# Performance work log

Hardware: AMD Instinct MI355X
Metric: run time of the kernel (lower is better)

The kernel has to match this reference:

```python
import jax, jax.numpy as jnp
import numpy as np

B, S, D, H = 2, 2048, 1024, 16
DK = D // H


def setup_inputs() -> dict:
    key = jax.random.key(0)
    ks = jax.random.split(key, 6)
    inp = {
        "mha_input": jax.random.normal(ks[0], (B, S, D), dtype=jnp.float32),
        "mask": jax.random.randint(ks[1], (B, S), 0, 2, dtype=jnp.int32),
        "Wq_w": jax.random.normal(ks[2], (D, D), dtype=jnp.float32) * 0.02,
        "Wq_b": jnp.zeros((D,), dtype=jnp.float32),
        "Wk_w": jax.random.normal(ks[3], (D, D), dtype=jnp.float32) * 0.02,
        "Wk_b": jnp.zeros((D,), dtype=jnp.float32),
        "Wv_w": jax.random.normal(ks[4], (D, D), dtype=jnp.float32) * 0.02,
        "Wv_b": jnp.zeros((D,), dtype=jnp.float32),
        "Wo_w": jax.random.normal(ks[5], (D, D), dtype=jnp.float32) * 0.02,
        "Wo_b": jnp.zeros((D,), dtype=jnp.float32),
    }
    return inp


def _mha(x, mask, Wq_w, Wq_b, Wk_w, Wk_b, Wv_w, Wv_b, Wo_w, Wo_b):
    b, s, d = x.shape
    # nn.Linear: x @ W.T + b
    q = (x @ Wq_w.T + Wq_b).reshape(b, s, H, DK).transpose(0, 2, 1, 3)  # [B,H,S,DK]
    k = (x @ Wk_w.T + Wk_b).reshape(b, s, H, DK).transpose(0, 2, 1, 3)
    v = (x @ Wv_w.T + Wv_b).reshape(b, s, H, DK).transpose(0, 2, 1, 3)
    scores = jnp.einsum("bhqd,bhkd->bhqk", q, k) / jnp.sqrt(jnp.float32(DK))
    # prefix mask: key columns < count_nonzero(mask[i]) are kept, rest -inf
    lengths = jnp.count_nonzero(mask, axis=1)                # [B]
    valid = jnp.arange(s)[None, :] < lengths[:, None]        # [B,S]
    scores = jnp.where(valid[:, None, None, :], scores, -jnp.inf)
    attn = jax.nn.softmax(scores, axis=-1)
    out = jnp.einsum("bhqk,bhkd->bhqd", attn, v)             # [B,H,S,DK]
    concat = out.transpose(0, 2, 1, 3).reshape(b, s, d)      # [B,S,D]
    return concat @ Wo_w.T + Wo_b


def reference(mha_input, mask, Wq_w, Wq_b, Wk_w, Wk_b, Wv_w, Wv_b, Wo_w, Wo_b):
    return _mha(mha_input, mask, Wq_w, Wq_b, Wk_w, Wk_b, Wv_w, Wv_b, Wo_w, Wo_b)
```

## Files before the change

### kernel.cpp

```cpp
#include <hip/hip_runtime.h>

using bf16x8 = __attribute__((ext_vector_type(8))) short;
using f32x4  = __attribute__((ext_vector_type(4))) float;

#define S_LEN 2048
#define NHEAD 16
#define DKH   64
#define HSZ   (S_LEN * DKH * 32)

__device__ __forceinline__ unsigned short f2bf(float x) {
  unsigned u = __builtin_bit_cast(unsigned, x);
  u += 0x7FFFu + ((u >> 16) & 1u);
  return (unsigned short)(u >> 16);
}

__device__ __forceinline__ void gload_lds16(const void* g, void* l) {
  __builtin_amdgcn_global_load_lds(
      (const __attribute__((address_space(1))) unsigned int*)g,
      (__attribute__((address_space(3))) unsigned int*)l, 16, 0, 0);
}

__global__ void cvt_kernel(const float* __restrict__ src,
                           unsigned short* __restrict__ dst, int n4) {
  int i = blockIdx.x * blockDim.x + threadIdx.x;
  if (i < n4) {
    float4 v = ((const float4*)src)[i];
    ushort4 o;
    o.x = f2bf(v.x); o.y = f2bf(v.y); o.z = f2bf(v.z); o.w = f2bf(v.w);
    ((ushort4*)dst)[i] = o;
  }
}

__global__ void lens_kernel(const int* __restrict__ mask, int* __restrict__ lens) {
  __shared__ int sred[256];
  const int b = blockIdx.x;
  int c = 0;
  for (int s = threadIdx.x; s < S_LEN; s += 256) c += (mask[b * S_LEN + s] != 0) ? 1 : 0;
  sred[threadIdx.x] = c;
  __syncthreads();
  for (int st = 128; st > 0; st >>= 1) {
    if (threadIdx.x < st) sred[threadIdx.x] += sred[threadIdx.x + st];
    __syncthreads();
  }
  if (threadIdx.x == 0) lens[b] = sred[0];
}

template <int MODE>
__global__ __launch_bounds__(256) void gemm_kernel(
    const unsigned short* __restrict__ A, const unsigned short* __restrict__ B,
    const float* __restrict__ b0, const float* __restrict__ b1,
    const float* __restrict__ b2, unsigned short* __restrict__ outQKV,
    float* __restrict__ outF, const int K) {
  __shared__ __align__(16) unsigned short As[128 * 32];
  __shared__ __align__(16) unsigned short Bs[128 * 32];
  const int tid = threadIdx.x;
  const int w = tid >> 6, lane = tid & 63;
  const int wm = w >> 1, wn = w & 1;
  const int r = lane & 15, g = lane >> 4;
  const int tm = blockIdx.y * 128, tn = blockIdx.x * 128;

  f32x4 acc[4][4] = {};
  const char* Ab = (const char*)A;
  const char* Bb = (const char*)B;
  char* AsB = (char*)As;
  char* BsB = (char*)Bs;

  for (int k0 = 0; k0 < K; k0 += 32) {
#pragma unroll
    for (int i = 0; i < 2; ++i) {
      const int o = (w * 2 + i) * 1024 + lane * 16;
      const int row = o >> 6, colb = o & 63;
      gload_lds16(Ab + ((size_t)(tm + row) * K + k0) * 2 + colb, AsB + (w * 2 + i) * 1024);
      gload_lds16(Bb + ((size_t)(tn + row) * K + k0) * 2 + colb, BsB + (w * 2 + i) * 1024);
    }
    __syncthreads();
    bf16x8 af[4], bfr[4];
#pragma unroll
    for (int mi = 0; mi < 4; ++mi)
      af[mi] = *(const bf16x8*)(AsB + (wm * 64 + mi * 16 + r) * 64 + g * 16);
#pragma unroll
    for (int ni = 0; ni < 4; ++ni)
      bfr[ni] = *(const bf16x8*)(BsB + (wn * 64 + ni * 16 + r) * 64 + g * 16);
#pragma unroll
    for (int mi = 0; mi < 4; ++mi)
#pragma unroll
      for (int ni = 0; ni < 4; ++ni)
        acc[mi][ni] = __builtin_amdgcn_mfma_f32_16x16x32_bf16(af[mi], bfr[ni], acc[mi][ni], 0, 0, 0);
    __syncthreads();
  }

  if (MODE == 0) {
    const int mat = tn >> 10;
    const float* bp = (mat == 0) ? b0 : (mat == 1) ? b1 : b2;
    const float scale = (mat == 0) ? 0.125f : 1.0f;
    unsigned short* dst = outQKV + (size_t)mat * HSZ;
#pragma unroll
    for (int mi = 0; mi < 4; ++mi)
#pragma unroll
      for (int ni = 0; ni < 4; ++ni)
#pragma unroll
        for (int reg = 0; reg < 4; ++reg) {
          const int m = tm + wm * 64 + mi * 16 + 4 * g + reg;
          const int n = tn + wn * 64 + ni * 16 + r;
          const int nn = n & 1023;
          const float v = (acc[mi][ni][reg] + bp[nn]) * scale;
          const int bI = m >> 11, s = m & 2047, hh = nn >> 6, dk = nn & 63;
          dst[(size_t)((bI * NHEAD + hh) * S_LEN + s) * DKH + dk] = f2bf(v);
        }
  } else {
#pragma unroll
    for (int mi = 0; mi < 4; ++mi)
#pragma unroll
      for (int ni = 0; ni < 4; ++ni)
#pragma unroll
        for (int reg = 0; reg < 4; ++reg) {
          const int m = tm + wm * 64 + mi * 16 + 4 * g + reg;
          const int n = tn + wn * 64 + ni * 16 + r;
          outF[(size_t)m * 1024 + n] = acc[mi][ni][reg] + b0[n];
        }
  }
}

__global__ __launch_bounds__(256) void attn_kernel(
    const unsigned short* __restrict__ qkv, const int* __restrict__ lens,
    unsigned short* __restrict__ outc) {
  __shared__ __align__(16) unsigned short Kt[64 * 64];
  __shared__ __align__(16) unsigned short Vt[64 * 64];
  __shared__ __align__(16) unsigned short Pl[4 * 16 * 64];
  const int tid = threadIdx.x;
  const int w = tid >> 6, lane = tid & 63;
  const int r = lane & 15, g = lane >> 4;
  const int bh = blockIdx.y;
  const int b = bh >> 4, h = bh & 15;
  const int q0 = blockIdx.x * 64;

  const unsigned short* Qp = qkv;
  const unsigned short* Kp = qkv + HSZ;
  const unsigned short* Vp = qkv + 2 * (size_t)HSZ;

  const size_t qbase = (size_t)(bh * S_LEN + q0 + w * 16 + r) * DKH;
  const bf16x8 qf0 = *(const bf16x8*)(Qp + qbase + g * 8);
  const bf16x8 qf1 = *(const bf16x8*)(Qp + qbase + 32 + g * 8);

  const int L = lens[b];
  const int nt = (L + 63) >> 6;
  float mrun = -__builtin_inff(), lrun = 0.f;
  f32x4 oacc[4] = {};

  char* KtB = (char*)Kt;
  char* VtB = (char*)Vt;
  char* PlB = (char*)Pl + w * 2048;
  const int swp = (r & 7) << 4;

  for (int t = 0; t < nt; ++t) {
    const int kv0 = t * 64;
    const char* kgb = (const char*)(Kp + (size_t)(bh * S_LEN + kv0) * DKH);
#pragma unroll
    for (int i = 0; i < 2; ++i) {
      const int o = i * 4096 + w * 1024 + lane * 16;
      const int row = o >> 7, colb = o & 127;
      gload_lds16(kgb + row * 128 + (colb ^ ((row & 7) << 4)), KtB + i * 4096 + w * 1024);
    }
    const unsigned short* vgb = Vp + (size_t)(bh * S_LEN + kv0) * DKH;
#pragma unroll
    for (int i = 0; i < 2; ++i) {
      const int u = i * 256 + tid;
      const int c = u & 63, g8 = u >> 6;
      const bf16x8 vv = *(const bf16x8*)(vgb + c * DKH + g8 * 8);
#pragma unroll
      for (int j = 0; j < 8; ++j) {
        const int dk = g8 * 8 + j;
        *(short*)(VtB + dk * 128 + ((2 * c) ^ ((dk & 7) << 4))) = vv[j];
      }
    }
    __syncthreads();

    f32x4 st[4];
#pragma unroll
    for (int f = 0; f < 4; ++f) {
      const int c = f * 16 + r;
      const int sw = (c & 7) << 4;
      const bf16x8 k0 = *(const bf16x8*)(KtB + c * 128 + ((g * 16) ^ sw));
      const bf16x8 k1 = *(const bf16x8*)(KtB + c * 128 + ((64 + g * 16) ^ sw));
      f32x4 a = {};
      a = __builtin_amdgcn_mfma_f32_16x16x32_bf16(k0, qf0, a, 0, 0, 0);
      a = __builtin_amdgcn_mfma_f32_16x16x32_bf16(k1, qf1, a, 0, 0, 0);
      st[f] = a;
    }
    if (t == nt - 1) {
#pragma unroll
      for (int f = 0; f < 4; ++f)
#pragma unroll
        for (int reg = 0; reg < 4; ++reg)
          if (kv0 + f * 16 + 4 * g + reg >= L) st[f][reg] = -__builtin_inff();
    }

    float mloc = st[0][0];
#pragma unroll
    for (int f = 0; f < 4; ++f)
#pragma unroll
      for (int reg = 0; reg < 4; ++reg) mloc = fmaxf(mloc, st[f][reg]);
    mloc = fmaxf(mloc, __shfl_xor(mloc, 16));
    mloc = fmaxf(mloc, __shfl_xor(mloc, 32));
    const float mnew = fmaxf(mrun, mloc);
    const float alpha = __expf(mrun - mnew);
    float psum = 0.f;
#pragma unroll
    for (int f = 0; f < 4; ++f)
#pragma unroll
      for (int reg = 0; reg < 4; ++reg) {
        const float p = __expf(st[f][reg] - mnew);
        st[f][reg] = p;
        psum += p;
      }
    psum += __shfl_xor(psum, 16);
    psum += __shfl_xor(psum, 32);
    lrun = lrun * alpha + psum;
    mrun = mnew;

    float areg[4];
#pragma unroll
    for (int reg = 0; reg < 4; ++reg) areg[reg] = __shfl(alpha, 4 * g + reg);
#pragma unroll
    for (int f = 0; f < 4; ++f)
#pragma unroll
      for (int reg = 0; reg < 4; ++reg) oacc[f][reg] *= areg[reg];

#pragma unroll
    for (int f = 0; f < 4; ++f) {
      ushort4 pw;
      pw.x = f2bf(st[f][0]); pw.y = f2bf(st[f][1]);
      pw.z = f2bf(st[f][2]); pw.w = f2bf(st[f][3]);
      *(ushort4*)(PlB + r * 128 + ((f * 32 + g * 8) ^ swp)) = pw;
    }

#pragma unroll
    for (int c2 = 0; c2 < 2; ++c2) {
      const bf16x8 pa = *(const bf16x8*)(PlB + r * 128 + ((c2 * 64 + g * 16) ^ swp));
#pragma unroll
      for (int f = 0; f < 4; ++f) {
        const int dk = f * 16 + r;
        const bf16x8 vf =
            *(const bf16x8*)(VtB + dk * 128 + ((c2 * 64 + g * 16) ^ ((dk & 7) << 4)));
        oacc[f] = __builtin_amdgcn_mfma_f32_16x16x32_bf16(pa, vf, oacc[f], 0, 0, 0);
      }
    }
    __syncthreads();
  }

  float lreg[4];
#pragma unroll
  for (int reg = 0; reg < 4; ++reg) lreg[reg] = __shfl(lrun, 4 * g + reg);
#pragma unroll
  for (int f = 0; f < 4; ++f) {
    const int dk = f * 16 + r;
#pragma unroll
    for (int reg = 0; reg < 4; ++reg) {
      const int row = 4 * g + reg;
      const float v = oacc[f][reg] / lreg[reg];
      outc[(size_t)(b * S_LEN + q0 + w * 16 + row) * 1024 + h * DKH + dk] = f2bf(v);
    }
  }
}

extern "C" void kernel_launch(void* const* d_in, const int* in_sizes, int n_in,
                              void* d_out, int out_size, void* d_ws, size_t ws_size,
                              hipStream_t stream) {
  const float* x  = (const float*)d_in[0];
  const int* mask = (const int*)d_in[1];
  const float* wq = (const float*)d_in[2];
  const float* bq = (const float*)d_in[3];
  const float* wk = (const float*)d_in[4];
  const float* bk = (const float*)d_in[5];
  const float* wv = (const float*)d_in[6];
  const float* bv = (const float*)d_in[7];
  const float* wo = (const float*)d_in[8];
  const float* bo = (const float*)d_in[9];
  (void)in_sizes; (void)n_in; (void)out_size; (void)ws_size;

  char* ws = (char*)d_ws;
  unsigned short* xb  = (unsigned short*)ws;
  unsigned short* wb  = (unsigned short*)(ws + 8388608);
  unsigned short* wob = (unsigned short*)(ws + 14680064);
  unsigned short* qkv = (unsigned short*)(ws + 16777216);
  unsigned short* ao  = (unsigned short*)(ws + 41943040);
  int* lens           = (int*)(ws + 50331648);
  float* out          = (float*)d_out;

  cvt_kernel<<<4096, 256, 0, stream>>>(x, xb, 1048576);
  cvt_kernel<<<1024, 256, 0, stream>>>(wq, wb, 262144);
  cvt_kernel<<<1024, 256, 0, stream>>>(wk, wb + 1048576, 262144);
  cvt_kernel<<<1024, 256, 0, stream>>>(wv, wb + 2097152, 262144);
  cvt_kernel<<<1024, 256, 0, stream>>>(wo, wob, 262144);
  lens_kernel<<<2, 256, 0, stream>>>(mask, lens);

  gemm_kernel<0><<<dim3(24, 32), 256, 0, stream>>>(xb, wb, bq, bk, bv, qkv, nullptr, 1024);
  attn_kernel<<<dim3(32, 32), 256, 0, stream>>>(qkv, lens, ao);
  gemm_kernel<1><<<dim3(8, 32), 256, 0, stream>>>(ao, wob, bo, nullptr, nullptr, nullptr, out, 1024);
}
```

Baseline: 227.9 us.

## Double-buffer K/V tiles, pre-transpose V in QKV GEMM, process 128 queries per block

The QKV projection now writes V transposed (dk-major), so the attention kernel can load V with async global-to-LDS copies instead of scalar transposing stores. K and V tiles are double-buffered so the next tile's load overlaps the current tile's compute. Each wave handles two 16-row query groups, which reuses K/V fragments and halves the grid. Softmax switches to exp2 with log2e folded into the Q scale, and s_setprio is raised around the MFMA sections. The costs are more LDS, more registers, and only 512 blocks, which lowers occupancy.

Result: faster. 216.6 us (-5.0%).

```diff
diff --git a/kernel.cpp b/kernel.cpp
--- a/kernel.cpp
+++ b/kernel.cpp
@@ -7,6 +7,13 @@
 #define NHEAD 16
 #define DKH   64
 #define HSZ   (S_LEN * DKH * 32)
+#define QSCALE 0.18033688011112042f
+
+#if __has_builtin(__builtin_amdgcn_exp2f)
+#define EXP2(x) __builtin_amdgcn_exp2f(x)
+#else
+#define EXP2(x) exp2f(x)
+#endif
 
 __device__ __forceinline__ unsigned short f2bf(float x) {
   unsigned u = __builtin_bit_cast(unsigned, x);
@@ -92,7 +99,7 @@
   if (MODE == 0) {
     const int mat = tn >> 10;
     const float* bp = (mat == 0) ? b0 : (mat == 1) ? b1 : b2;
-    const float scale = (mat == 0) ? 0.125f : 1.0f;
+    const float scale = (mat == 0) ? QSCALE : 1.0f;
     unsigned short* dst = outQKV + (size_t)mat * HSZ;
 #pragma unroll
     for (int mi = 0; mi < 4; ++mi)
@@ -105,7 +112,11 @@
           const int nn = n & 1023;
           const float v = (acc[mi][ni][reg] + bp[nn]) * scale;
           const int bI = m >> 11, s = m & 2047, hh = nn >> 6, dk = nn & 63;
-          dst[(size_t)((bI * NHEAD + hh) * S_LEN + s) * DKH + dk] = f2bf(v);
+          if (mat == 2) {
+            dst[(size_t)((bI * NHEAD + hh) * DKH + dk) * S_LEN + s] = f2bf(v);
+          } else {
+            dst[(size_t)((bI * NHEAD + hh) * S_LEN + s) * DKH + dk] = f2bf(v);
+          }
         }
   } else {
 #pragma unroll
@@ -121,144 +132,182 @@
   }
 }
 
+__device__ __forceinline__ void online_sm(f32x4* st, float& mrun, float& lrun,
+                                          f32x4* oacc, int g) {
+  float mloc = st[0][0];
+#pragma unroll
+  for (int f = 0; f < 4; ++f)
+#pragma unroll
+    for (int q = 0; q < 4; ++q) mloc = fmaxf(mloc, st[f][q]);
+  mloc = fmaxf(mloc, __shfl_xor(mloc, 16));
+  mloc = fmaxf(mloc, __shfl_xor(mloc, 32));
+  const float mnew = fmaxf(mrun, mloc);
+  const float alpha = EXP2(mrun - mnew);
+  mrun = mnew;
+  float psum = 0.f;
+#pragma unroll
+  for (int f = 0; f < 4; ++f)
+#pragma unroll
+    for (int q = 0; q < 4; ++q) {
+      const float p = EXP2(st[f][q] - mnew);
+      st[f][q] = p;
+      psum += p;
+    }
+  psum += __shfl_xor(psum, 16);
+  psum += __shfl_xor(psum, 32);
+  lrun = lrun * alpha + psum;
+  float areg[4];
+#pragma unroll
+  for (int q = 0; q < 4; ++q) areg[q] = __shfl(alpha, 4 * g + q);
+#pragma unroll
+  for (int f = 0; f < 4; ++f)
+#pragma unroll
+    for (int q = 0; q < 4; ++q) oacc[f][q] *= areg[q];
+}
+
 __global__ __launch_bounds__(256) void attn_kernel(
     const unsigned short* __restrict__ qkv, const int* __restrict__ lens,
     unsigned short* __restrict__ outc) {
-  __shared__ __align__(16) unsigned short Kt[64 * 64];
-  __shared__ __align__(16) unsigned short Vt[64 * 64];
-  __shared__ __align__(16) unsigned short Pl[4 * 16 * 64];
+  __shared__ __align__(16) unsigned short Kt[2][4096];
+  __shared__ __align__(16) unsigned short Vt[2][4096];
+  __shared__ __align__(16) unsigned short Pl[4][2][1024];
   const int tid = threadIdx.x;
   const int w = tid >> 6, lane = tid & 63;
   const int r = lane & 15, g = lane >> 4;
   const int bh = blockIdx.y;
   const int b = bh >> 4, h = bh & 15;
-  const int q0 = blockIdx.x * 64;
+  const int q0 = blockIdx.x * 128;
 
   const unsigned short* Qp = qkv;
   const unsigned short* Kp = qkv + HSZ;
-  const unsigned short* Vp = qkv + 2 * (size_t)HSZ;
-
-  const size_t qbase = (size_t)(bh * S_LEN + q0 + w * 16 + r) * DKH;
-  const bf16x8 qf0 = *(const bf16x8*)(Qp + qbase + g * 8);
-  const bf16x8 qf1 = *(const bf16x8*)(Qp + qbase + 32 + g * 8);
+  const unsigned short* VTp = qkv + 2 * (size_t)HSZ;
+
+  const size_t qbase = (size_t)(bh * S_LEN + q0 + w * 32 + r) * DKH;
+  const bf16x8 qa0 = *(const bf16x8*)(Qp + qbase + g * 8);
+  const bf16x8 qa1 = *(const bf16x8*)(Qp + qbase + 32 + g * 8);
+  const bf16x8 qb0 = *(const bf16x8*)(Qp + qbase + 16 * DKH + g * 8);
+  const bf16x8 qb1 = *(const bf16x8*)(Qp + qbase + 16 * DKH + 32 + g * 8);
 
   const int L = lens[b];
   const int nt = (L + 63) >> 6;
-  float mrun = -__builtin_inff(), lrun = 0.f;
-  f32x4 oacc[4] = {};
-
-  char* KtB = (char*)Kt;
-  char* VtB = (char*)Vt;
-  char* PlB = (char*)Pl + w * 2048;
+  float mA = -__builtin_inff(), lA = 0.f;
+  float mB = -__builtin_inff(), lB = 0.f;
+  f32x4 oA[4] = {}, oB[4] = {};
+
+  char* PA = (char*)Pl[w][0];
+  char* PB = (char*)Pl[w][1];
   const int swp = (r & 7) << 4;
 
-  for (int t = 0; t < nt; ++t) {
-    const int kv0 = t * 64;
-    const char* kgb = (const char*)(Kp + (size_t)(bh * S_LEN + kv0) * DKH);
+  const char* kgb0 = (const char*)(Kp + (size_t)bh * S_LEN * DKH);
+  const char* vgb0 = (const char*)(VTp + (size_t)bh * DKH * S_LEN);
+
+  auto stage = [&](int tt, int bb) {
+    const char* kgb = kgb0 + (size_t)tt * 64 * DKH * 2;
+    const char* vgb = vgb0 + (size_t)tt * 64 * 2;
+    char* kd = (char*)Kt[bb];
+    char* vd = (char*)Vt[bb];
 #pragma unroll
     for (int i = 0; i < 2; ++i) {
       const int o = i * 4096 + w * 1024 + lane * 16;
       const int row = o >> 7, colb = o & 127;
-      gload_lds16(kgb + row * 128 + (colb ^ ((row & 7) << 4)), KtB + i * 4096 + w * 1024);
-    }
-    const unsigned short* vgb = Vp + (size_t)(bh * S_LEN + kv0) * DKH;
-#pragma unroll
-    for (int i = 0; i < 2; ++i) {
-      const int u = i * 256 + tid;
-      const int c = u & 63, g8 = u >> 6;
-      const bf16x8 vv = *(const bf16x8*)(vgb + c * DKH + g8 * 8);
-#pragma unroll
-      for (int j = 0; j < 8; ++j) {
-        const int dk = g8 * 8 + j;
-        *(short*)(VtB + dk * 128 + ((2 * c) ^ ((dk & 7) << 4))) = vv[j];
-      }
-    }
-    __syncthreads();
-
-    f32x4 st[4];
+      const int cs = colb ^ ((row & 7) << 4);
+      gload_lds16(kgb + row * 128 + cs, kd + i * 4096 + w * 1024);
+      gload_lds16(vgb + (size_t)row * (S_LEN * 2) + cs, vd + i * 4096 + w * 1024);
+    }
+  };
+
+  if (nt > 0) stage(0, 0);
+  __syncthreads();
+
+  int buf = 0;
+  for (int t = 0; t < nt; ++t) {
+    if (t + 1 < nt) stage(t + 1, buf ^ 1);
+
+    const char* KtB = (const char*)Kt[buf];
+    f32x4 sa[4], sb[4];
+    __builtin_amdgcn_s_setprio(1);
 #pragma unroll
     for (int f = 0; f < 4; ++f) {
       const int c = f * 16 + r;
       const int sw = (c & 7) << 4;
       const bf16x8 k0 = *(const bf16x8*)(KtB + c * 128 + ((g * 16) ^ sw));
       const bf16x8 k1 = *(const bf16x8*)(KtB + c * 128 + ((64 + g * 16) ^ sw));
-      f32x4 a = {};
-      a = __builtin_amdgcn_mfma_f32_16x16x32_bf16(k0, qf0, a, 0, 0, 0);
-      a = __builtin_amdgcn_mfma_f32_16x16x32_bf16(k1, qf1, a, 0, 0, 0);
-      st[f] = a;
-    }
+      f32x4 x = {};
+      x = __builtin_amdgcn_mfma_f32_16x16x32_bf16(k0, qa0, x, 0, 0, 0);
+      x = __builtin_amdgcn_mfma_f32_16x16x32_bf16(k1, qa1, x, 0, 0, 0);
+      sa[f] = x;
+      f32x4 y = {};
+      y = __builtin_amdgcn_mfma_f32_16x16x32_bf16(k0, qb0, y, 0, 0, 0);
+      y = __builtin_amdgcn_mfma_f32_16x16x32_bf16(k1, qb1, y, 0, 0, 0);
+      sb[f] = y;
+    }
+    __builtin_amdgcn_s_setprio(0);
+
+    const int kv0 = t * 64;
     if (t == nt - 1) {
 #pragma unroll
       for (int f = 0; f < 4; ++f)
 #pragma unroll
-        for (int reg = 0; reg < 4; ++reg)
-          if (kv0 + f * 16 + 4 * g + reg >= L) st[f][reg] = -__builtin_inff();
-    }
-
-    float mloc = st[0][0];
-#pragma unroll
-    for (int f = 0; f < 4; ++f)
-#pragma unroll
-      for (int reg = 0; reg < 4; ++reg) mloc = fmaxf(mloc, st[f][reg]);
-    mloc = fmaxf(mloc, __shfl_xor(mloc, 16));
-    mloc = fmaxf(mloc, __shfl_xor(mloc, 32));
-    const float mnew = fmaxf(mrun, mloc);
-    const float alpha = __expf(mrun - mnew);
-    float psum = 0.f;
-#pragma unroll
-    for (int f = 0; f < 4; ++f)
-#pragma unroll
-      for (int reg = 0; reg < 4; ++reg) {
-        const float p = __expf(st[f][reg] - mnew);
-        st[f][reg] = p;
-        psum += p;
-      }
-    psum += __shfl_xor(psum, 16);
-    psum += __shfl_xor(psum, 32);
-    lrun = lrun * alpha + psum;
-    mrun = mnew;
-
-    float areg[4];
-#pragma unroll
-    for (int reg = 0; reg < 4; ++reg) areg[reg] = __shfl(alpha, 4 * g + reg);
-#pragma unroll
-    for (int f = 0; f < 4; ++f)
-#pragma unroll
-      for (int reg = 0; reg < 4; ++reg) oacc[f][reg] *= areg[reg];
+        for (int q = 0; q < 4; ++q)
+          if (kv0 + f * 16 + 4 * g + q >= L) {
+            sa[f][q] = -__builtin_inff();
+            sb[f][q] = -__builtin_inff();
+          }
+    }
+
+    online_sm(sa, mA, lA, oA, g);
+    online_sm(sb, mB, lB, oB, g);
 
 #pragma unroll
     for (int f = 0; f < 4; ++f) {
       ushort4 pw;
-      pw.x = f2bf(st[f][0]); pw.y = f2bf(st[f][1]);
-      pw.z = f2bf(st[f][2]); pw.w = f2bf(st[f][3]);
-      *(ushort4*)(PlB + r * 128 + ((f * 32 + g * 8) ^ swp)) = pw;
-    }
-
+      pw.x = f2bf(sa[f][0]); pw.y = f2bf(sa[f][1]);
+      pw.z = f2bf(sa[f][2]); pw.w = f2bf(sa[f][3]);
+      *(ushort4*)(PA + r * 128 + ((f * 32 + g * 8) ^ swp)) = pw;
+      ushort4 qw;
+      qw.x = f2bf(sb[f][0]); qw.y = f2bf(sb[f][1]);
+      qw.z = f2bf(sb[f][2]); qw.w = f2bf(sb[f][3]);
+      *(ushort4*)(PB + r * 128 + ((f * 32 + g * 8) ^ swp)) = qw;
+    }
+
+    const char* VtB = (const char*)Vt[buf];
 #pragma unroll
     for (int c2 = 0; c2 < 2; ++c2) {
-      const bf16x8 pa = *(const bf16x8*)(PlB + r * 128 + ((c2 * 64 + g * 16) ^ swp));
+      const bf16x8 pa = *(const bf16x8*)(PA + r * 128 + ((c2 * 64 + g * 16) ^ swp));
+      const bf16x8 pb = *(const bf16x8*)(PB + r * 128 + ((c2 * 64 + g * 16) ^ swp));
+      __builtin_amdgcn_s_setprio(1);
 #pragma unroll
       for (int f = 0; f < 4; ++f) {
         const int dk = f * 16 + r;
         const bf16x8 vf =
             *(const bf16x8*)(VtB + dk * 128 + ((c2 * 64 + g * 16) ^ ((dk & 7) << 4)));
-        oacc[f] = __builtin_amdgcn_mfma_f32_16x16x32_bf16(pa, vf, oacc[f], 0, 0, 0);
+        oA[f] = __builtin_amdgcn_mfma_f32_16x16x32_bf16(pa, vf, oA[f], 0, 0, 0);
+        oB[f] = __builtin_amdgcn_mfma_f32_16x16x32_bf16(pb, vf, oB[f], 0, 0, 0);
       }
-    }
+      __builtin_amdgcn_s_setprio(0);
+    }
+
     __syncthreads();
-  }
-
-  float lreg[4];
-#pragma unroll
-  for (int reg = 0; reg < 4; ++reg) lreg[reg] = __shfl(lrun, 4 * g + reg);
+    buf ^= 1;
+  }
+
+  const float iA = 1.0f / lA;
+  const float iB = 1.0f / lB;
+  float rA[4], rB[4];
+#pragma unroll
+  for (int q = 0; q < 4; ++q) {
+    rA[q] = __shfl(iA, 4 * g + q);
+    rB[q] = __shfl(iB, 4 * g + q);
+  }
 #pragma unroll
   for (int f = 0; f < 4; ++f) {
     const int dk = f * 16 + r;
 #pragma unroll
-    for (int reg = 0; reg < 4; ++reg) {
-      const int row = 4 * g + reg;
-      const float v = oacc[f][reg] / lreg[reg];
-      outc[(size_t)(b * S_LEN + q0 + w * 16 + row) * 1024 + h * DKH + dk] = f2bf(v);
+    for (int q = 0; q < 4; ++q) {
+      const int rowA = q0 + w * 32 + 4 * g + q;
+      outc[(size_t)(b * S_LEN + rowA) * 1024 + h * DKH + dk] = f2bf(oA[f][q] * rA[q]);
+      const int rowB = rowA + 16;
+      outc[(size_t)(b * S_LEN + rowB) * 1024 + h * DKH + dk] = f2bf(oB[f][q] * rB[q]);
     }
   }
 }
@@ -295,6 +344,6 @@
   lens_kernel<<<2, 256, 0, stream>>>(mask, lens);
 
   gemm_kernel<0><<<dim3(24, 32), 256, 0, stream>>>(xb, wb, bq, bk, bv, qkv, nullptr, 1024);
-  attn_kernel<<<dim3(32, 32), 256, 0, stream>>>(qkv, lens, ao);
+  attn_kernel<<<dim3(16, 32), 256, 0, stream>>>(qkv, lens, ao);
   gemm_kernel<1><<<dim3(8, 32), 256, 0, stream>>>(ao, wob, bo, nullptr, nullptr, nullptr, out, 1024);
 }
```
